# Kernel tuning notes

Measured on AMD Instinct MI355X. Metric: run time of the kernel, lower is better.

Reference implementation:

```python
import jax, jax.numpy as jnp
import numpy as np

VOCAB = 128000; D = 128; H = 4; HD = D // H; NL = 2; DOUT = 64
MAXW = 32; B = 64; L = 64; N_ITERS = 32

def _ln(x, g, b):
    m = jnp.mean(x, -1, keepdims=True)
    v = jnp.var(x, -1, keepdims=True)
    return (x - m) * jax.lax.rsqrt(v + 1e-5) * g + b

def _encoder(x, pad, p):
    # post-norm torch TransformerEncoderLayer, relu activation. x: [N,W,D], pad True=padding key
    neg = jnp.where(pad, -1e9, 0.0)[:, None, None, :]
    n = x.shape[0]
    for l in range(NL):
        qkv = x @ p["Wqkv"][l].T + p["bqkv"][l]
        q, k, v = jnp.split(qkv, 3, axis=-1)
        q = q.reshape(n, MAXW, H, HD).transpose(0, 2, 1, 3)
        k = k.reshape(n, MAXW, H, HD).transpose(0, 2, 1, 3)
        v = v.reshape(n, MAXW, H, HD).transpose(0, 2, 1, 3)
        s = jnp.einsum('nhqd,nhkd->nhqk', q, k) * (1.0 / float(np.sqrt(HD))) + neg
        o = jnp.einsum('nhqk,nhkd->nhqd', jax.nn.softmax(s, -1), v)
        o = o.transpose(0, 2, 1, 3).reshape(n, MAXW, D) @ p["Wo"][l].T + p["bo"][l]
        x = _ln(x + o, p["ln1g"][l], p["ln1b"][l])
        f = jax.nn.relu(x @ p["W1"][l].T + p["b1"][l]) @ p["W2"][l].T + p["b2"][l]
        x = _ln(x + f, p["ln2g"][l], p["ln2b"][l])
    return x

def _forward(p, token_ids, padding_mask, key):
    seq_len = jnp.sum(~padding_mask, 1).astype(jnp.int32)
    pos_idx = jnp.arange(MAXW)
    bidx = jnp.arange(B)

    def _head(x, W1h, b1h, W2h, b2h):
        return (jax.nn.relu(x @ W1h.T + b1h) @ W2h.T + b2h)[:, 0]

    def _gru(x, h):
        gi = x @ p["gru_Wih"].T + p["gru_bih"]
        gh = h @ p["gru_Whh"].T + p["gru_bhh"]
        ir, iz, inn = jnp.split(gi, 3, -1)
        hr, hz, hn = jnp.split(gh, 3, -1)
        r = jax.nn.sigmoid(ir + hr)
        z = jax.nn.sigmoid(iz + hz)
        return (1.0 - z) * jnp.tanh(inn + r * hn) + z * h

    def step(carry, k):
        win_ids, win_len, input_pos, gru_h, done = carry
        active = ~done
        pad = ~((pos_idx[None, :] < win_len[:, None]) & active[:, None])
        pad = pad.at[:, 0].set(False)  # keep softmax finite for empty windows; t1 zeroed below
        x = p["tok_emb"][win_ids] + p["pos_emb"][None, :, :]
        enc = _encoder(x, pad, p)
        last = enc[bidx, jnp.maximum(win_len - 1, 0)]
        vec = last @ p["proj_W"].T + p["proj_b"]
        vec = vec / jnp.maximum(jnp.linalg.norm(vec, axis=-1, keepdims=True), 1e-12)
        nonempty = (win_len > 0) & active
        t1 = jnp.where(nonempty[:, None], vec, 0.0)
        gru_h = jnp.where(active[:, None], _gru(t1, gru_h), gru_h)
        has_input = active & (input_pos < seq_len)
        nt = token_ids[bidx, jnp.clip(input_pos, 0, L - 1)]
        next_embs = jnp.where(has_input[:, None], p["tok_emb"][nt], 0.0)
        acc_l = _head(jnp.concatenate([next_embs, t1, gru_h], 1), p["acc_W1"], p["acc_b1"], p["acc_W2"], p["acc_b2"])
        tg = jnp.concatenate([t1, gru_h], 1)
        emt_l = _head(tg, p["emt_W1"], p["emt_b1"], p["emt_W2"], p["emt_b2"])
        evt_l = _head(tg, p["evt_W1"], p["evt_b1"], p["evt_W2"], p["evt_b2"])
        k1, k2, k3 = jax.random.split(k, 3)
        acc_s = jax.random.bernoulli(k1, jax.nn.sigmoid(acc_l))
        emt_s = jax.random.bernoulli(k2, jax.nn.sigmoid(emt_l))
        evt_s = jax.random.bernoulli(k3, jax.nn.sigmoid(evt_l))
        lp = jnp.stack([jax.nn.log_sigmoid(jnp.where(acc_s, acc_l, -acc_l)),
                        jax.nn.log_sigmoid(jnp.where(emt_s, emt_l, -emt_l)),
                        jax.nn.log_sigmoid(jnp.where(evt_s, evt_l, -evt_l))], 1)
        dec = jnp.stack([acc_s, emt_s, evt_s], 1).astype(jnp.float32)
        a = acc_s & has_input
        e = emt_s & nonempty
        v = evt_s & nonempty
        none = active & ~(a | e | v)
        a = a | (none & has_input)
        e = e | (none & ~has_input & (win_len > 0))
        a_eff = a & (win_len < MAXW)
        win_ids = jnp.where(a_eff[:, None] & (pos_idx[None, :] == win_len[:, None]), nt[:, None], win_ids)
        input_pos = input_pos + a_eff.astype(jnp.int32)
        win_len = win_len + a_eff.astype(jnp.int32)
        emit_event = e & (win_len > 0)
        v_eff = v & (win_len > 0)
        win_ids = jnp.where(v_eff[:, None], jnp.roll(win_ids, -1, axis=1), win_ids)
        win_len = win_len - v_eff.astype(jnp.int32)
        done = done | (active & (input_pos >= seq_len) & (win_len == 0))
        return (win_ids, win_len, input_pos, gru_h, done), (t1, lp, dec, emit_event)

    init = (jnp.zeros((B, MAXW), dtype=token_ids.dtype), jnp.zeros(B, jnp.int32), jnp.zeros(B, jnp.int32),
            jnp.zeros((B, D), jnp.float32), seq_len == 0)
    keys = jax.random.split(key, N_ITERS)
    _, (t1s, lps, decs, emits) = jax.lax.scan(step, init, keys)
    return t1s, lps, decs, jnp.sum(emits.astype(jnp.int32), 0)

def setup_inputs():
    key = jax.random.key(0)
    ks = jax.random.split(key, 20)
    def rn(k, shape):
        return jax.random.normal(k, shape, jnp.float32) * 0.02
    inp = {}
    inp["token_ids"] = jax.random.randint(ks[0], (B, L), 0, VOCAB)
    inp["padding_mask"] = jnp.zeros((B, L), dtype=bool)
    inp["token_instr_idx"] = jax.random.randint(ks[1], (B, L), 0, 32)
    inp["n_instructions"] = jax.random.randint(ks[2], (B,), 1, 32)
    inp["tok_emb"] = rn(ks[3], (VOCAB, D))
    inp["pos_emb"] = rn(ks[4], (MAXW, D))
    inp["Wqkv"] = rn(ks[5], (NL, 3 * D, D)); inp["bqkv"] = jnp.zeros((NL, 3 * D))
    inp["Wo"] = rn(ks[6], (NL, D, D)); inp["bo"] = jnp.zeros((NL, D))
    inp["ln1g"] = jnp.ones((NL, D)); inp["ln1b"] = jnp.zeros((NL, D))
    inp["W1"] = rn(ks[7], (NL, 4 * D, D)); inp["b1"] = jnp.zeros((NL, 4 * D))
    inp["W2"] = rn(ks[8], (NL, D, 4 * D)); inp["b2"] = jnp.zeros((NL, D))
    inp["ln2g"] = jnp.ones((NL, D)); inp["ln2b"] = jnp.zeros((NL, D))
    inp["proj_W"] = rn(ks[9], (DOUT, D)); inp["proj_b"] = jnp.zeros((DOUT,))
    inp["gru_Wih"] = rn(ks[10], (3 * D, DOUT)); inp["gru_Whh"] = rn(ks[11], (3 * D, D))
    inp["gru_bih"] = jnp.zeros((3 * D,)); inp["gru_bhh"] = jnp.zeros((3 * D,))
    inp["acc_W1"] = rn(ks[12], (D, 2 * D + DOUT)); inp["acc_b1"] = jnp.zeros((D,))
    inp["acc_W2"] = rn(ks[13], (1, D)); inp["acc_b2"] = jnp.full((1,), 2.0)
    inp["emt_W1"] = rn(ks[14], (D, D + DOUT)); inp["emt_b1"] = jnp.zeros((D,))
    inp["emt_W2"] = rn(ks[15], (1, D)); inp["emt_b2"] = jnp.full((1,), -2.0)
    inp["evt_W1"] = rn(ks[16], (D, D + DOUT)); inp["evt_b1"] = jnp.zeros((D,))
    inp["evt_W2"] = rn(ks[17], (1, D)); inp["evt_b2"] = jnp.full((1,), -2.0)
    return inp

def reference(token_ids, padding_mask, token_instr_idx, n_instructions, tok_emb, pos_emb, Wqkv, bqkv, Wo, bo, ln1g, ln1b, W1, b1, W2, b2, ln2g, ln2b, proj_W, proj_b, gru_Wih, gru_Whh, gru_bih, gru_bhh, acc_W1, acc_b1, acc_W2, acc_b2, emt_W1, emt_b1, emt_W2, emt_b2, evt_W1, evt_b1, evt_W2, evt_b2):
    p = dict(tok_emb=tok_emb, pos_emb=pos_emb, Wqkv=Wqkv, bqkv=bqkv, Wo=Wo, bo=bo, ln1g=ln1g, ln1b=ln1b,
             W1=W1, b1=b1, W2=W2, b2=b2, ln2g=ln2g, ln2b=ln2b, proj_W=proj_W, proj_b=proj_b,
             gru_Wih=gru_Wih, gru_Whh=gru_Whh, gru_bih=gru_bih, gru_bhh=gru_bhh,
             acc_W1=acc_W1, acc_b1=acc_b1, acc_W2=acc_W2, acc_b2=acc_b2,
             emt_W1=emt_W1, emt_b1=emt_b1, emt_W2=emt_W2, emt_b2=emt_b2,
             evt_W1=evt_W1, evt_b1=evt_b1, evt_W2=evt_W2, evt_b2=evt_b2)
    # token_instr_idx / n_instructions are only used for emission bookkeeping (no tensor math); unused here.
    return _forward(p, token_ids, padding_mask, jax.random.key(42))
```

## Files before the change

### kernel.cpp

```cpp
#include <hip/hip_runtime.h>
#include <hip/hip_bf16.h>


#define XS 132
#define QS 388
#define HS 516
#define PS 36
#define NW 16

struct KParams {
  const int* token_ids;
  const unsigned char* pad;
  const void *tok_emb, *pos_emb, *Wqkv, *bqkv, *Wo, *bo, *ln1g, *ln1b;
  const void *W1, *b1, *W2, *b2, *ln2g, *ln2b, *projW, *projb;
  const void *gWih, *gWhh, *gbih, *gbhh;
  const void *accW1, *accb1, *accW2, *accb2;
  const void *emtW1, *emtb1, *emtW2, *emtb2;
  const void *evtW1, *evtb1, *evtW2, *evtb2;
  float* out;
};

struct Smem {
  float xbuf[32 * XS];
  float qh[32 * HS];
  float obuf[32 * XS];
  float pbuf[4608];
  float attT[128];
  float tva[128];
  double gild[384];
  double ghld[384];
  double hsd[128];
  double t1d[64];
  double catd[320];
  double hid2d[384];
  double logitsd[3];
  int win_ids[32];
  int sI[6];
  unsigned keyts[32][2];
};

__device__ __forceinline__ float ldw(const float* p){ return *p; }
__device__ __forceinline__ float ldw(const unsigned short* p){
  return __uint_as_float(((unsigned)*p) << 16);
}
__device__ __forceinline__ float4 ld4(const float* p){ return *(const float4*)p; }
__device__ __forceinline__ float4 ld4(const unsigned short* p){
  ushort4 u = *(const ushort4*)p;
  return make_float4(__uint_as_float((unsigned)u.x << 16),
                     __uint_as_float((unsigned)u.y << 16),
                     __uint_as_float((unsigned)u.z << 16),
                     __uint_as_float((unsigned)u.w << 16));
}
template<typename WT>
__device__ __forceinline__ double ldwd(const WT* p){ return (double)ldw(p); }

__device__ __forceinline__ float temb(const void* te, int isb, long long idx){
  if (isb) return __uint_as_float(((unsigned)((const unsigned short*)te)[idx]) << 16);
  return ((const float*)te)[idx];
}

__device__ __forceinline__ void tfry(unsigned k0, unsigned k1, unsigned x0, unsigned x1,
                                     unsigned &o0, unsigned &o1){
  unsigned ks2 = k0 ^ k1 ^ 0x1BD11BDAu;
  unsigned x = x0 + k0, y = x1 + k1;
#define TFR(r) { x += y; y = (y << r) | (y >> (32 - r)); y ^= x; }
  TFR(13) TFR(15) TFR(26) TFR(6)  x += k1;  y += ks2 + 1u;
  TFR(17) TFR(29) TFR(16) TFR(24) x += ks2; y += k0 + 2u;
  TFR(13) TFR(15) TFR(26) TFR(6)  x += k0;  y += k1 + 3u;
  TFR(17) TFR(29) TFR(16) TFR(24) x += k1;  y += ks2 + 4u;
  TFR(13) TFR(15) TFR(26) TFR(6)  x += ks2; y += k0 + 5u;
#undef TFR
  o0 = x; o1 = y;
}
__device__ __forceinline__ float u01(unsigned bits){
  return __uint_as_float((bits >> 9) | 0x3f800000u) - 1.0f;
}
__device__ __forceinline__ double logsigd(double x){
  return fmin(x, 0.0) - log1p(exp(-fabs(x)));
}
__device__ __forceinline__ float wredsum(float v, int width){
  for (int m = width >> 1; m > 0; m >>= 1) v += __shfl_xor(v, m, width);
  return v;
}
__device__ __forceinline__ double wredsumd(double v, int width){
  for (int m = width >> 1; m > 0; m >>= 1) v += __shfl_xor(v, m, width);
  return v;
}
__device__ __forceinline__ float dot4f(float4 a, float4 b){
  return a.x*b.x + a.y*b.y + a.z*b.z + a.w*b.w;
}

template<int T, int K, bool RELU, typename WT>
__device__ void gemm_tok(const WT* __restrict__ Wm, const WT* __restrict__ bias,
                         int J, const float* __restrict__ xl, int xs,
                         float* __restrict__ ol, int os, int ntok,
                         int lane, int wv, int nwv)
{
  const int JBG = J >> 6;
  const int ntt = (ntok + T - 1) / T;
  for (int item = wv; item < JBG * ntt; item += nwv) {
    const int jg = item % JBG, tt = item / JBG;
    const int j0 = jg * 64 + lane;
    float acc[T];
#pragma unroll
    for (int t = 0; t < T; ++t) acc[t] = 0.f;
    const float* xr = xl + tt * T * xs;
    const WT* wr = Wm + (size_t)j0 * K;
#pragma unroll 4
    for (int k = 0; k < K; k += 4) {
      float4 w = ld4(wr + k);
      float4 xv[T];
#pragma unroll
      for (int t = 0; t < T; ++t) xv[t] = *(const float4*)(xr + t * xs + k);
#pragma unroll
      for (int t = 0; t < T; ++t)
        acc[t] += w.x * xv[t].x + w.y * xv[t].y + w.z * xv[t].z + w.w * xv[t].w;
    }
    float bj = ldw(bias + j0);
#pragma unroll
    for (int t = 0; t < T; ++t) {
      int tok = tt * T + t;
      if (tok < ntok) {
        float v = acc[t] + bj;
        if (RELU) v = fmaxf(v, 0.f);
        ol[tok * os + j0] = v;
      }
    }
  }
}

template<int K, typename WT>
__device__ __forceinline__ float dotgf(const WT* __restrict__ w, const float* x){
  float acc = 0.f;
#pragma unroll 8
  for (int k = 0; k < K; k += 4) {
    float4 wv = ld4(w + k);
    acc += wv.x * x[k] + wv.y * x[k+1] + wv.z * x[k+2] + wv.w * x[k+3];
  }
  return acc;
}
template<int K, typename WT>
__device__ __forceinline__ double dotgd(const WT* __restrict__ w, const double* x){
  double acc = 0.0;
#pragma unroll 8
  for (int k = 0; k < K; k += 4) {
    float4 wv = ld4(w + k);
    acc += (double)wv.x * x[k] + (double)wv.y * x[k+1]
         + (double)wv.z * x[k+2] + (double)wv.w * x[k+3];
  }
  return acc;
}
template<int K, typename WT>
__device__ __forceinline__ double dotgdx(const WT* __restrict__ w, const float* x){
  double acc = 0.0;
#pragma unroll 8
  for (int k = 0; k < K; k += 4) {
    float4 wv = ld4(w + k);
    acc += (double)wv.x * (double)x[k] + (double)wv.y * (double)x[k+1]
         + (double)wv.z * (double)x[k+2] + (double)wv.w * (double)x[k+3];
  }
  return acc;
}

template<typename WT>
__device__ void ln_rows(float* xb, const float* ob, const WT* __restrict__ g,
                        const WT* __restrict__ bb, int W, int tid){
  if (tid >= 256) return;
  const int i = tid >> 3, sub = tid & 7;
  const int base = i * XS + sub * 16;
  float y[16];
  float s = 0.f;
#pragma unroll
  for (int u = 0; u < 16; u += 4) {
    float4 xv = *(const float4*)(xb + base + u);
    float4 ov = *(const float4*)(ob + base + u);
    y[u] = xv.x + ov.x; y[u+1] = xv.y + ov.y; y[u+2] = xv.z + ov.z; y[u+3] = xv.w + ov.w;
    s += y[u] + y[u+1] + y[u+2] + y[u+3];
  }
  s = wredsum(s, 8);
  const float m = s * (1.0f / 128.0f);
  float vs = 0.f;
#pragma unroll
  for (int u = 0; u < 16; ++u) { float d = y[u] - m; vs += d * d; }
  vs = wredsum(vs, 8);
  const float rstd = 1.0f / sqrtf(vs * (1.0f / 128.0f) + 1e-5f);
  if (i < W) {
#pragma unroll
    for (int u = 0; u < 16; u += 4) {
      float4 gg = ld4(g + sub * 16 + u);
      float4 bv = ld4(bb + sub * 16 + u);
      float4 r;
      r.x = (y[u]   - m) * rstd * gg.x + bv.x;
      r.y = (y[u+1] - m) * rstd * gg.y + bv.y;
      r.z = (y[u+2] - m) * rstd * gg.z + bv.z;
      r.w = (y[u+3] - m) * rstd * gg.w + bv.w;
      *(float4*)(xb + base + u) = r;
    }
  }
}
template<typename WT>
__device__ __forceinline__ void ln_tail(float* xrow, const float* add,
                                        const WT* __restrict__ g,
                                        const WT* __restrict__ bb, int tid){
  if (tid < 64) {
    float y0 = xrow[tid] + add[tid];
    float y1 = xrow[64 + tid] + add[64 + tid];
    float m = wredsum(y0 + y1, 64) * (1.0f / 128.0f);
    float d0 = y0 - m, d1 = y1 - m;
    float rstd = 1.0f / sqrtf(wredsum(d0 * d0 + d1 * d1, 64) * (1.0f / 128.0f) + 1e-5f);
    xrow[tid] = d0 * rstd * ldw(g + tid) + ldw(bb + tid);
    xrow[64 + tid] = d1 * rstd * ldw(g + 64 + tid) + ldw(bb + 64 + tid);
  }
}

template<typename WT>
__device__ void run_all(const KParams& P, Smem& S, int row, int tid, int isbEmb){
  const WT* tok_embw = (const WT*)P.tok_emb;
  const WT* pos_emb = (const WT*)P.pos_emb;
  const WT* Wqkv = (const WT*)P.Wqkv;   const WT* bqkv = (const WT*)P.bqkv;
  const WT* Wo = (const WT*)P.Wo;       const WT* bo = (const WT*)P.bo;
  const WT* ln1g = (const WT*)P.ln1g;   const WT* ln1b = (const WT*)P.ln1b;
  const WT* W1 = (const WT*)P.W1;       const WT* b1 = (const WT*)P.b1;
  const WT* W2 = (const WT*)P.W2;       const WT* b2 = (const WT*)P.b2;
  const WT* ln2g = (const WT*)P.ln2g;   const WT* ln2b = (const WT*)P.ln2b;
  const WT* projW = (const WT*)P.projW; const WT* projb = (const WT*)P.projb;
  const WT* gWih = (const WT*)P.gWih;   const WT* gWhh = (const WT*)P.gWhh;
  const WT* gbih = (const WT*)P.gbih;   const WT* gbhh = (const WT*)P.gbhh;
  const WT* accW1 = (const WT*)P.accW1; const WT* accb1 = (const WT*)P.accb1;
  const WT* accW2 = (const WT*)P.accW2; const WT* accb2 = (const WT*)P.accb2;
  const WT* emtW1 = (const WT*)P.emtW1; const WT* emtb1 = (const WT*)P.emtb1;
  const WT* emtW2 = (const WT*)P.emtW2; const WT* emtb2 = (const WT*)P.emtb2;
  const WT* evtW1 = (const WT*)P.evtW1; const WT* evtb1 = (const WT*)P.evtb1;
  const WT* evtW2 = (const WT*)P.evtW2; const WT* evtb2 = (const WT*)P.evtb2;

  const int lane = tid & 63, wid = tid >> 6;

  if (tid == 0) {
    int seq = 0;
    for (int l = 0; l < 64; ++l) seq += (P.pad[row * 64 + l] == 0);
    S.sI[0] = 0; S.sI[1] = 0; S.sI[2] = (seq == 0) ? 1 : 0; S.sI[3] = seq; S.sI[4] = 0;
  }
  if (tid < 128) S.hsd[tid] = 0.0;
  if (tid < 32) {
    S.win_ids[tid] = 0;
    unsigned a0, a1;
    tfry(0u, 42u, 0u, (unsigned)tid, a0, a1);
    S.keyts[tid][0] = a0; S.keyts[tid][1] = a1;
  }
  __syncthreads();

  for (int t = 0; t < 32; ++t) {
    const int wl = S.sI[0], ip = S.sI[1], done = S.sI[2], seq = S.sI[3];
    const int act = !done;
    const int W = wl;
    const int enc = (act && wl > 0) ? 1 : 0;
    const int jl = (W > 0) ? (W - 1) : 0;

    if (enc) {
      for (int idx = tid; idx < W * 16; idx += 1024) {
        int i = idx >> 4, d0 = (idx & 15) << 3;
        const WT* te = tok_embw + (long long)S.win_ids[i] * 128 + d0;
        const WT* pe = pos_emb + (size_t)i * 128 + d0;
        float4 t0 = ld4(te), t1 = ld4(te + 4), p0 = ld4(pe), p1 = ld4(pe + 4);
        float* dst = &S.xbuf[i * XS + d0];
        float4 r0, r1;
        r0.x = t0.x + p0.x; r0.y = t0.y + p0.y; r0.z = t0.z + p0.z; r0.w = t0.w + p0.w;
        r1.x = t1.x + p1.x; r1.y = t1.y + p1.y; r1.z = t1.z + p1.z; r1.w = t1.w + p1.w;
        *(float4*)dst = r0;
        *(float4*)(dst + 4) = r1;
      }
      __syncthreads();
      gemm_tok<8, 128, false>(Wqkv, bqkv, 384, S.xbuf, XS, S.qh, QS, W, lane, wid, NW);
      __syncthreads();
      if (tid < 128) {
        int h = tid >> 5, i = tid & 31;
        if (i < W) {
          float4 q[8];
#pragma unroll
          for (int kk = 0; kk < 8; ++kk) q[kk] = *(const float4*)&S.qh[i * QS + h * 32 + kk * 4];
          int pb = (h * 32 + i) * PS;
          float m = -1e30f;
          for (int j = 0; j < W; ++j) {
            float s = 0.f;
#pragma unroll
            for (int kk = 0; kk < 8; ++kk)
              s += dot4f(q[kk], *(const float4*)&S.qh[j * QS + 128 + h * 32 + kk * 4]);
            s *= 0.17677669529663687f;
            S.pbuf[pb + j] = s;
            m = fmaxf(m, s);
          }
          float sum = 0.f;
          for (int j = 0; j < W; ++j) { float e = expf(S.pbuf[pb + j] - m); S.pbuf[pb + j] = e; sum += e; }
          float rs = 1.0f / sum;
          for (int j = 0; j < W; ++j) S.pbuf[pb + j] *= rs;
        }
      }
      __syncthreads();
      {
        int c = tid & 127, qsub = tid >> 7, h = c >> 5;
        for (int i = qsub; i < W; i += 8) {
          float acc = 0.f;
          for (int j = 0; j < W; ++j) acc += S.pbuf[(h * 32 + i) * PS + j] * S.qh[j * QS + 256 + c];
          S.obuf[i * XS + c] = acc;
        }
      }
      __syncthreads();
      gemm_tok<4, 128, false>(Wo, bo, 128, S.obuf, XS, S.pbuf, XS, W, lane, wid, NW);
      __syncthreads();
      ln_rows(S.xbuf, S.pbuf, ln1g, ln1b, W, tid);
      __syncthreads();
      gemm_tok<8, 128, true>(W1, b1, 512, S.xbuf, XS, S.qh, HS, W, lane, wid, NW);
      __syncthreads();
      gemm_tok<8, 512, false>(W2, b2, 128, S.qh, HS, S.obuf, XS, W, lane, wid, NW);
      __syncthreads();
      ln_rows(S.xbuf, S.obuf, ln2g, ln2b, W, tid);
      __syncthreads();
      {
        const WT* Wq = Wqkv + 384 * 128;
        const WT* bq = bqkv + 384;
        if (wid < 14) {
          gemm_tok<8, 128, false>(Wq + 128 * 128, bq + 128, 256,
                                  S.xbuf, XS, S.qh + 128, QS, W, lane, wid, 14);
        } else {
          int j = tid - 896;
          S.qh[jl * QS + j] = ldw(bq + j) + dotgf<128>(Wq + j * 128, &S.xbuf[jl * XS]);
        }
        __syncthreads();
        if (tid < 128) {
          int h = tid >> 5, j = tid & 31;
          float s = -1e30f;
          if (j < W) {
            s = 0.f;
#pragma unroll
            for (int kk = 0; kk < 8; ++kk)
              s += dot4f(*(const float4*)&S.qh[jl * QS + h * 32 + kk * 4],
                         *(const float4*)&S.qh[j * QS + 128 + h * 32 + kk * 4]);
            s *= 0.17677669529663687f;
          }
          float m = s;
          for (int mk = 16; mk; mk >>= 1) m = fmaxf(m, __shfl_xor(m, mk, 32));
          float e = (j < W) ? expf(s - m) : 0.f;
          float sum = e;
          for (int mk = 16; mk; mk >>= 1) sum += __shfl_xor(sum, mk, 32);
          if (j < W) S.pbuf[h * PS + j] = e * (1.0f / sum);
        }
        __syncthreads();
        if (tid < 128) {
          int h = tid >> 5;
          float acc = 0.f;
          for (int j = 0; j < W; ++j) acc += S.pbuf[h * PS + j] * S.qh[j * QS + 256 + tid];
          S.attT[tid] = acc;
        }
        __syncthreads();
        if (tid < 512) {
          int j = tid >> 2, q = tid & 3;
          float v = dotgf<32>(Wo + 16384 + (size_t)j * 128 + q * 32, S.attT + q * 32);
          v += __shfl_xor(v, 1, 64);
          v += __shfl_xor(v, 2, 64);
          if (q == 0) S.tva[j] = ldw(bo + 128 + j) + v;
        }
        __syncthreads();
        ln_tail(&S.xbuf[jl * XS], S.tva, ln1g + 128, ln1b + 128, tid);
        __syncthreads();
        {
          int j = tid >> 1, h = tid & 1;
          float v = dotgf<64>(W1 + (size_t)(512 + j) * 128 + h * 64, &S.xbuf[jl * XS] + h * 64);
          v += __shfl_xor(v, 1, 64);
          if (h == 0) S.qh[j] = fmaxf(ldw(b1 + 512 + j) + v, 0.f);
        }
        __syncthreads();
        if (tid < 512) {
          int j = tid >> 2, q = tid & 3;
          float v = dotgf<128>(W2 + (size_t)(128 + j) * 512 + q * 128, S.qh + q * 128);
          v += __shfl_xor(v, 1, 64);
          v += __shfl_xor(v, 2, 64);
          if (q == 0) S.tva[j] = ldw(b2 + 128 + j) + v;
        }
        __syncthreads();
        ln_tail(&S.xbuf[jl * XS], S.tva, ln2g + 128, ln2b + 128, tid);
        __syncthreads();
      }
    }

    if (tid < 64) {
      double tv = 0.0;
      if (enc) {
        double v = ldwd(projb + tid) + dotgdx<128>(projW + tid * 128, &S.xbuf[jl * XS]);
        double ss = wredsumd(v * v, 64);
        tv = v / fmax(sqrt(ss), 1e-12);
      }
      S.t1d[tid] = tv;
      S.catd[128 + tid] = tv;
      P.out[(size_t)t * 4096 + row * 64 + tid] = (float)tv;
    } else if (tid >= 128 && tid < 896) {
      if (act) {
        int jj = tid - 128;
        int j = jj >> 1, h = jj & 1;
        double v = dotgd<64>(gWhh + (size_t)j * 128 + h * 64, S.hsd + h * 64);
        v += __shfl_xor(v, 1, 64);
        if (h == 0) S.ghld[j] = ldwd(gbhh + j) + v;
      }
    } else if (tid >= 896) {
      int j = tid - 896;
      int ipc = ip < 0 ? 0 : (ip > 63 ? 63 : ip);
      int nt = P.token_ids[row * 64 + ipc];
      int has_in = (act && (ip < seq)) ? 1 : 0;
      S.catd[j] = has_in ? (double)temb(P.tok_emb, isbEmb, (long long)nt * 128 + j) : 0.0;
    }
    __syncthreads();

    if (act) {
      if (tid < 768) {
        int j = tid >> 1, h = tid & 1;
        double v = dotgd<32>(gWih + (size_t)j * 64 + h * 32, S.t1d + h * 32);
        v += __shfl_xor(v, 1, 64);
        if (h == 0) S.gild[j] = ldwd(gbih + j) + v;
      }
      __syncthreads();
    }

    if (tid < 128) {
      if (act) {
        double r = 1.0 / (1.0 + exp(-(S.gild[tid] + S.ghld[tid])));
        double z = 1.0 / (1.0 + exp(-(S.gild[128 + tid] + S.ghld[128 + tid])));
        double n = tanh(S.gild[256 + tid] + r * S.ghld[256 + tid]);
        S.hsd[tid] = (1.0 - z) * n + z * S.hsd[tid];
      }
      S.catd[192 + tid] = S.hsd[tid];
    }
    __syncthreads();

    if (tid < 768) {
      int jo = tid >> 1, h = tid & 1;
      double v;
      if (jo < 128) {
        v = dotgd<160>(accW1 + (size_t)jo * 320 + h * 160, S.catd + h * 160);
      } else if (jo < 256) {
        int j = jo - 128;
        v = dotgd<96>(emtW1 + (size_t)j * 192 + h * 96, S.catd + 128 + h * 96);
      } else {
        int j = jo - 256;
        v = dotgd<96>(evtW1 + (size_t)j * 192 + h * 96, S.catd + 128 + h * 96);
      }
      v += __shfl_xor(v, 1, 64);
      if (h == 0) {
        double b = (jo < 128) ? ldwd(accb1 + jo)
                 : (jo < 256 ? ldwd(emtb1 + jo - 128) : ldwd(evtb1 + jo - 256));
        S.hid2d[jo] = fmax(b + v, 0.0);
      }
    }
    __syncthreads();

    {
      int hw = tid >> 6;
      if (hw < 3) {
        int ln = tid & 63;
        const WT* w2 = (hw == 0) ? accW2 : ((hw == 1) ? emtW2 : evtW2);
        const WT* b2p = (hw == 0) ? accb2 : ((hw == 1) ? emtb2 : evtb2);
        double pp = S.hid2d[hw * 128 + ln] * ldwd(w2 + ln)
                  + S.hid2d[hw * 128 + 64 + ln] * ldwd(w2 + 64 + ln);
        pp = wredsumd(pp, 64);
        if (ln == 0) S.logitsd[hw] = pp + ldwd(b2p);
      }
    }
    __syncthreads();

    if (tid < 64) {
      unsigned k0 = S.keyts[t][0], k1 = S.keyts[t][1];
      int smp_l = 0;
      if (tid < 3) {
        double lgv = S.logitsd[tid];
        unsigned sk0, sk1, r0, r1;
        tfry(k0, k1, 0u, (unsigned)tid, sk0, sk1);
        tfry(sk0, sk1, 0u, (unsigned)row, r0, r1);
        double u = (double)u01(r0 ^ r1);
        double p = 1.0 / (1.0 + exp(-lgv));
        smp_l = (u < p) ? 1 : 0;
        P.out[131072 + (size_t)t * 192 + row * 3 + tid] = (float)logsigd(smp_l ? lgv : -lgv);
        P.out[137216 + (size_t)t * 192 + row * 3 + tid] = smp_l ? 1.0f : 0.0f;
      }
      int sa = __shfl(smp_l, 0, 64);
      int se = __shfl(smp_l, 1, 64);
      int sv = __shfl(smp_l, 2, 64);
      if (tid == 0) {
        int wl2 = wl, ip2 = ip, dn = done;
        int nonempty = (wl2 > 0) && act;
        int has_in = act && (ip2 < seq);
        int a = sa && has_in;
        int e = se && nonempty;
        int v = sv && nonempty;
        int none = act && !(a || e || v);
        a = a || (none && has_in);
        e = e || (none && !has_in && (wl2 > 0));
        int aeff = a && (wl2 < 32);
        int ipc = ip2 < 0 ? 0 : (ip2 > 63 ? 63 : ip2);
        int nt = P.token_ids[row * 64 + ipc];
        if (aeff) { S.win_ids[wl2] = nt; ip2 += 1; wl2 += 1; }
        int emit = e && (wl2 > 0);
        S.sI[4] += emit;
        int veff = v && (wl2 > 0);
        if (veff) {
          int w0 = S.win_ids[0];
#pragma unroll
          for (int i2 = 0; i2 < 31; ++i2) S.win_ids[i2] = S.win_ids[i2 + 1];
          S.win_ids[31] = w0;
          wl2 -= 1;
        }
        if (act && (ip2 >= seq) && (wl2 == 0)) dn = 1;
        S.sI[0] = wl2; S.sI[1] = ip2; S.sI[2] = dn;
      }
    }
    __syncthreads();
  }
  if (tid == 0) P.out[143360 + row] = (float)S.sI[4];
}

__global__ __launch_bounds__(1024, 4) void src_main_kernel(KParams P){
  __shared__ __align__(16) Smem S;
  const int row = blockIdx.x;
  const int tid = threadIdx.x;
  const bool isb = (((const unsigned short*)P.ln1g)[0] == (unsigned short)0x3F80);
  if (isb) run_all<unsigned short>(P, S, row, tid, 1);
  else     run_all<float>(P, S, row, tid, 0);
}

extern "C" void kernel_launch(void* const* d_in, const int* in_sizes, int n_in,
                              void* d_out, int out_size, void* d_ws, size_t ws_size,
                              hipStream_t stream) {
  KParams P;
  P.token_ids = (const int*)d_in[0];
  P.pad = (const unsigned char*)d_in[1];
  P.tok_emb = d_in[4];  P.pos_emb = d_in[5];
  P.Wqkv = d_in[6];     P.bqkv = d_in[7];
  P.Wo = d_in[8];       P.bo = d_in[9];
  P.ln1g = d_in[10];    P.ln1b = d_in[11];
  P.W1 = d_in[12];      P.b1 = d_in[13];
  P.W2 = d_in[14];      P.b2 = d_in[15];
  P.ln2g = d_in[16];    P.ln2b = d_in[17];
  P.projW = d_in[18];   P.projb = d_in[19];
  P.gWih = d_in[20];    P.gWhh = d_in[21];
  P.gbih = d_in[22];    P.gbhh = d_in[23];
  P.accW1 = d_in[24];   P.accb1 = d_in[25];
  P.accW2 = d_in[26];   P.accb2 = d_in[27];
  P.emtW1 = d_in[28];   P.emtb1 = d_in[29];
  P.emtW2 = d_in[30];   P.emtb2 = d_in[31];
  P.evtW1 = d_in[32];   P.evtb1 = d_in[33];
  P.evtW2 = d_in[34];   P.evtb2 = d_in[35];
  P.out = (float*)d_out;
  hipLaunchKernelGGL(src_main_kernel, dim3(64), dim3(1024), 0, stream, P);
}
```

Measured before the change: 4.564 ms.

## Store V transposed in shared memory and vectorize attention PV with split softmax

The QKV GEMM epilogue now writes the V part into a transposed shared buffer (vT), so the attention-times-V loops read contiguous float4 rows of P and V, with padding lanes zeroed. The score and softmax stage now uses two threads per query row combined via shuffles, which doubles the active threads. Several GEMM token-tile sizes drop from 8 to 4 to raise parallelism for small windows. This costs extra LDS space and strided, bank-conflicting scalar stores into vT.

```diff
diff --git a/kernel.cpp b/kernel.cpp
--- a/kernel.cpp
+++ b/kernel.cpp
@@ -6,6 +6,7 @@
 #define QS 388
 #define HS 516
 #define PS 36
+#define VS 36
 #define NW 16
 
 struct KParams {
@@ -25,6 +26,7 @@
   float qh[32 * HS];
   float obuf[32 * XS];
   float pbuf[4608];
+  float vT[128 * VS];
   float attT[128];
   float tva[128];
   double gild[384];
@@ -90,11 +92,11 @@
   return a.x*b.x + a.y*b.y + a.z*b.z + a.w*b.w;
 }
 
-template<int T, int K, bool RELU, typename WT>
+template<int T, int K, bool RELU, int VOFF, typename WT>
 __device__ void gemm_tok(const WT* __restrict__ Wm, const WT* __restrict__ bias,
                          int J, const float* __restrict__ xl, int xs,
                          float* __restrict__ ol, int os, int ntok,
-                         int lane, int wv, int nwv)
+                         int lane, int wv, int nwv, float* __restrict__ vt)
 {
   const int JBG = J >> 6;
   const int ntt = (ntok + T - 1) / T;
@@ -123,7 +125,8 @@
       if (tok < ntok) {
         float v = acc[t] + bj;
         if (RELU) v = fmaxf(v, 0.f);
-        ol[tok * os + j0] = v;
+        if (VOFF >= 0 && j0 >= VOFF) vt[(j0 - VOFF) * VS + tok] = v;
+        else                         ol[tok * os + j0] = v;
       }
     }
   }
@@ -247,6 +250,7 @@
     tfry(0u, 42u, 0u, (unsigned)tid, a0, a1);
     S.keyts[tid][0] = a0; S.keyts[tid][1] = a1;
   }
+  for (int idx = tid; idx < 128 * VS; idx += 1024) S.vT[idx] = 0.f;
   __syncthreads();
 
   for (int t = 0; t < 32; ++t) {
@@ -255,6 +259,7 @@
     const int W = wl;
     const int enc = (act && wl > 0) ? 1 : 0;
     const int jl = (W > 0) ? (W - 1) : 0;
+    const int Wp4 = (W + 3) & ~3;
 
     if (enc) {
       for (int idx = tid; idx < W * 16; idx += 1024) {
@@ -270,17 +275,20 @@
         *(float4*)(dst + 4) = r1;
       }
       __syncthreads();
-      gemm_tok<8, 128, false>(Wqkv, bqkv, 384, S.xbuf, XS, S.qh, QS, W, lane, wid, NW);
-      __syncthreads();
-      if (tid < 128) {
-        int h = tid >> 5, i = tid & 31;
+      gemm_tok<4, 128, false, 256>(Wqkv, bqkv, 384, S.xbuf, XS, S.qh, QS, W, lane, wid, NW, S.vT);
+      __syncthreads();
+      if (tid < 256) {
+        int r = tid >> 1, half = tid & 1;
+        int h = r >> 5, i = r & 31;
         if (i < W) {
           float4 q[8];
 #pragma unroll
           for (int kk = 0; kk < 8; ++kk) q[kk] = *(const float4*)&S.qh[i * QS + h * 32 + kk * 4];
-          int pb = (h * 32 + i) * PS;
+          const int pb = r * PS;
+          const int j0 = half * 16;
+          const int j1 = (j0 + 16 < W) ? (j0 + 16) : W;
           float m = -1e30f;
-          for (int j = 0; j < W; ++j) {
+          for (int j = j0; j < j1; ++j) {
             float s = 0.f;
 #pragma unroll
             for (int kk = 0; kk < 8; ++kk)
@@ -289,29 +297,43 @@
             S.pbuf[pb + j] = s;
             m = fmaxf(m, s);
           }
+          m = fmaxf(m, __shfl_xor(m, 1, 64));
           float sum = 0.f;
-          for (int j = 0; j < W; ++j) { float e = expf(S.pbuf[pb + j] - m); S.pbuf[pb + j] = e; sum += e; }
+          for (int j = j0; j < j1; ++j) {
+            float e = expf(S.pbuf[pb + j] - m);
+            S.pbuf[pb + j] = e;
+            sum += e;
+          }
+          sum += __shfl_xor(sum, 1, 64);
           float rs = 1.0f / sum;
-          for (int j = 0; j < W; ++j) S.pbuf[pb + j] *= rs;
+          for (int j = j0; j < j1; ++j) S.pbuf[pb + j] *= rs;
+          for (int j = W + half; j < Wp4; j += 2) S.pbuf[pb + j] = 0.f;
         }
       }
       __syncthreads();
       {
-        int c = tid & 127, qsub = tid >> 7, h = c >> 5;
-        for (int i = qsub; i < W; i += 8) {
+        int c = tid & 127, g = tid >> 7;
+        int h = c >> 5;
+        const float* vrow = &S.vT[c * VS];
+        for (int i = g; i < W; i += 8) {
+          const float* prow = &S.pbuf[(h * 32 + i) * PS];
           float acc = 0.f;
-          for (int j = 0; j < W; ++j) acc += S.pbuf[(h * 32 + i) * PS + j] * S.qh[j * QS + 256 + c];
+          for (int j4 = 0; j4 < W; j4 += 4) {
+            float4 p = *(const float4*)(prow + j4);
+            float4 v = *(const float4*)(vrow + j4);
+            acc += p.x * v.x + p.y * v.y + p.z * v.z + p.w * v.w;
+          }
           S.obuf[i * XS + c] = acc;
         }
       }
       __syncthreads();
-      gemm_tok<4, 128, false>(Wo, bo, 128, S.obuf, XS, S.pbuf, XS, W, lane, wid, NW);
+      gemm_tok<4, 128, false, -1>(Wo, bo, 128, S.obuf, XS, S.pbuf, XS, W, lane, wid, NW, S.vT);
       __syncthreads();
       ln_rows(S.xbuf, S.pbuf, ln1g, ln1b, W, tid);
       __syncthreads();
-      gemm_tok<8, 128, true>(W1, b1, 512, S.xbuf, XS, S.qh, HS, W, lane, wid, NW);
-      __syncthreads();
-      gemm_tok<8, 512, false>(W2, b2, 128, S.qh, HS, S.obuf, XS, W, lane, wid, NW);
+      gemm_tok<8, 128, true, -1>(W1, b1, 512, S.xbuf, XS, S.qh, HS, W, lane, wid, NW, S.vT);
+      __syncthreads();
+      gemm_tok<4, 512, false, -1>(W2, b2, 128, S.qh, HS, S.obuf, XS, W, lane, wid, NW, S.vT);
       __syncthreads();
       ln_rows(S.xbuf, S.obuf, ln2g, ln2b, W, tid);
       __syncthreads();
@@ -319,8 +341,8 @@
         const WT* Wq = Wqkv + 384 * 128;
         const WT* bq = bqkv + 384;
         if (wid < 14) {
-          gemm_tok<8, 128, false>(Wq + 128 * 128, bq + 128, 256,
-                                  S.xbuf, XS, S.qh + 128, QS, W, lane, wid, 14);
+          gemm_tok<4, 128, false, 128>(Wq + 128 * 128, bq + 128, 256,
+                                       S.xbuf, XS, S.qh + 128, QS, W, lane, wid, 14, S.vT);
         } else {
           int j = tid - 896;
           S.qh[jl * QS + j] = ldw(bq + j) + dotgf<128>(Wq + j * 128, &S.xbuf[jl * XS]);
@@ -343,12 +365,19 @@
           float sum = e;
           for (int mk = 16; mk; mk >>= 1) sum += __shfl_xor(sum, mk, 32);
           if (j < W) S.pbuf[h * PS + j] = e * (1.0f / sum);
+          else       S.pbuf[h * PS + j] = 0.f;
         }
         __syncthreads();
         if (tid < 128) {
           int h = tid >> 5;
+          const float* prow = &S.pbuf[h * PS];
+          const float* vrow = &S.vT[tid * VS];
           float acc = 0.f;
-          for (int j = 0; j < W; ++j) acc += S.pbuf[h * PS + j] * S.qh[j * QS + 256 + tid];
+          for (int j4 = 0; j4 < W; j4 += 4) {
+            float4 p = *(const float4*)(prow + j4);
+            float4 v = *(const float4*)(vrow + j4);
+            acc += p.x * v.x + p.y * v.y + p.z * v.z + p.w * v.w;
+          }
           S.attT[tid] = acc;
         }
         __syncthreads();
```

Measured after the change: 4.966 ms. +8.8%, slower.
